# Optimization experiments

Hardware: AMD Instinct MI355X
Metric: run time of the kernel (lower is better)

## Reference

```python
import jax, jax.numpy as jnp
import numpy as np

B = 8          # batch samples (decomposition_permutations)
M = 100000     # points per sample
V = 100000     # coarse voxels for max-pool/unpool (stride scaler groups)


def setup_inputs() -> dict:
    key = jax.random.key(0)
    ks = jax.random.split(key, 6)
    N = B * M
    C_in, C = 128, 128
    fea = jax.random.normal(ks[0], (N, C_in), jnp.float32)
    W1 = jax.random.normal(ks[1], (C_in, C), jnp.float32) / np.sqrt(C_in).astype(np.float32)
    b1 = jnp.zeros((C,), jnp.float32)
    W2 = jax.random.normal(ks[2], (C, 1), jnp.float32) / np.sqrt(C).astype(np.float32)
    b2 = jnp.zeros((1,), jnp.float32)
    voxel_ids = jax.random.randint(ks[3], (N,), 0, V, jnp.int32)
    target_idx = jax.random.randint(ks[4], (N // 2,), 0, N, jnp.int32)
    return dict(fea=fea, W1=W1, b1=b1, W2=W2, b2=b2,
                voxel_ids=voxel_ids, target_idx=target_idx, target_num=M // 2)


def _get_keep(p, voxel_ids, target_num):
    # MinkowskiMaxPooling + PoolingTranspose diff: per-voxel max broadcast back
    local_max = jax.ops.segment_max(p, voxel_ids, num_segments=V)[voxel_ids]
    local_max_mask = p != local_max  # points NOT equal to their local max
    pm = p.reshape(B, M)
    mm = local_max_mask.reshape(B, M)
    # kthvalue over masked values per sample: k = M - target_num (1-indexed)
    vals = jnp.where(mm, pm, jnp.inf)          # non-masked pushed to the end
    k = M - target_num
    thr = jnp.sort(vals, axis=1)[:, k - 1]     # [B] per-sample thresholds
    keep = pm > thr[:, None]                   # BCE branch: keep pred > threshold
    keep = keep | ~mm                          # keep.logical_or_(~local_max_mask)
    return keep.reshape(B * M)


def reference(fea, W1, b1, W2, b2, voxel_ids, target_idx, target_num):
    # upsample_block -> classify_block
    h = jax.nn.relu(fea @ W1 + b1)             # [N, C]
    pred = h @ W2 + b2                         # [N, 1]
    p = pred[:, 0]
    keep = _get_keep(p, voxel_ids, target_num)
    # get_target: kernel_map scatter -> keep_target (training: keep |= keep_target)
    keep_target = jnp.zeros((p.shape[0],), bool).at[target_idx].set(True)
    keep = keep | keep_target
    # MinkowskiPruning (mask instead of compaction to keep shapes static)
    out = h * keep[:, None].astype(h.dtype)
    return out, pred, keep_target
```

## Files before the change

### kernel.cpp

```cpp
#include <hip/hip_runtime.h>
#include <stdint.h>

#define BATCH 8
#define C 128
#define TPB 256
#define GEMM_BLOCKS 512
#define TILE_R 128
#define HGRID 2048

__device__ __forceinline__ unsigned f2key(float f){
  unsigned b = __float_as_uint(f);
  return (b & 0x80000000u) ? ~b : (b | 0x80000000u);
}

__global__ __launch_bounds__(TPB, 1) void k_gemm(
    const float* __restrict__ fea, const float* __restrict__ W1,
    const float* __restrict__ b1, const float* __restrict__ W2,
    const float* __restrict__ b2, const int* __restrict__ vox,
    float* __restrict__ out, float* __restrict__ pred,
    unsigned* __restrict__ segkey, int N)
{
  __shared__ float sW1t[C * C];
  __shared__ double sPredS[2 * TILE_R];

  const int tid  = threadIdx.x;
  const int lane = tid & 63;
  const int wid  = tid >> 6;
  const int wr   = wid >> 1;
  const int wc   = wid & 1;
  const int rowoff = wr * 64 + (lane >> 3) * 8;
  const int coloff = wc * 64 + (lane & 7) * 8;
  const int lmask  = lane & 7;

  for (int idx = tid; idx < C * C; idx += TPB) {
    int k = idx >> 7, c = idx & 127;
    sW1t[c * C + (((k >> 2) ^ ((c >> 3) & 7)) << 2) + (k & 3)] = W1[idx];
  }
  float b1v[8];
  #pragma unroll
  for (int i = 0; i < 8; ++i) b1v[i] = b1[coloff + i];
  const double b2d = (double)b2[0];
  __syncthreads();

  const int nTiles = N / TILE_R;
  const float* bcol = &sW1t[coloff * C];

  for (int tile = blockIdx.x; tile < nTiles; tile += GEMM_BLOCKS) {
    const size_t trow = (size_t)tile * TILE_R;
    const float* abase = fea + (trow + rowoff) * C;

    float4 Aa[8], Ab[8];
    #pragma unroll
    for (int j = 0; j < 8; ++j) Aa[j] = *(const float4*)(abase + j * C);

    float acc[8][8];
    #pragma unroll
    for (int j = 0; j < 8; ++j)
      #pragma unroll
      for (int i = 0; i < 8; ++i) acc[j][i] = b1v[i];

    #pragma unroll 1
    for (int kg = 0; kg < 32; kg += 2) {
      #pragma unroll
      for (int j = 0; j < 8; ++j)
        Ab[j] = *(const float4*)(abase + j * C + (kg + 1) * 4);
      {
        const int goff = ((kg ^ lmask) << 2);
        float4 Bv[8];
        #pragma unroll
        for (int i = 0; i < 8; ++i)
          Bv[i] = *(const float4*)(bcol + i * C + goff);
        #pragma unroll
        for (int j = 0; j < 8; ++j) {
          #pragma unroll
          for (int i = 0; i < 8; ++i) acc[j][i] = fmaf(Aa[j].x, Bv[i].x, acc[j][i]);
          #pragma unroll
          for (int i = 0; i < 8; ++i) acc[j][i] = fmaf(Aa[j].y, Bv[i].y, acc[j][i]);
          #pragma unroll
          for (int i = 0; i < 8; ++i) acc[j][i] = fmaf(Aa[j].z, Bv[i].z, acc[j][i]);
          #pragma unroll
          for (int i = 0; i < 8; ++i) acc[j][i] = fmaf(Aa[j].w, Bv[i].w, acc[j][i]);
        }
      }
      if (kg + 2 < 32) {
        #pragma unroll
        for (int j = 0; j < 8; ++j)
          Aa[j] = *(const float4*)(abase + j * C + (kg + 2) * 4);
      }
      {
        const int goff = (((kg + 1) ^ lmask) << 2);
        float4 Bv[8];
        #pragma unroll
        for (int i = 0; i < 8; ++i)
          Bv[i] = *(const float4*)(bcol + i * C + goff);
        #pragma unroll
        for (int j = 0; j < 8; ++j) {
          #pragma unroll
          for (int i = 0; i < 8; ++i) acc[j][i] = fmaf(Ab[j].x, Bv[i].x, acc[j][i]);
          #pragma unroll
          for (int i = 0; i < 8; ++i) acc[j][i] = fmaf(Ab[j].y, Bv[i].y, acc[j][i]);
          #pragma unroll
          for (int i = 0; i < 8; ++i) acc[j][i] = fmaf(Ab[j].z, Bv[i].z, acc[j][i]);
          #pragma unroll
          for (int i = 0; i < 8; ++i) acc[j][i] = fmaf(Ab[j].w, Bv[i].w, acc[j][i]);
        }
      }
    }

    float w2f[8];
    #pragma unroll
    for (int i = 0; i < 8; ++i) w2f[i] = W2[coloff + i];
    double pdv[8];
    #pragma unroll
    for (int j = 0; j < 8; ++j) {
      float hv[8];
      #pragma unroll
      for (int i = 0; i < 8; ++i) hv[i] = fmaxf(acc[j][i], 0.f);
      const size_t row = trow + rowoff + j;
      *(float4*)(out + row * C + coloff)     = make_float4(hv[0], hv[1], hv[2], hv[3]);
      *(float4*)(out + row * C + coloff + 4) = make_float4(hv[4], hv[5], hv[6], hv[7]);
      double pd = 0.0;
      #pragma unroll
      for (int i = 0; i < 8; ++i) pd += (double)hv[i] * (double)w2f[i];
      pdv[j] = pd;
    }
    #pragma unroll
    for (int j = 0; j < 8; ++j) {
      double pd = pdv[j];
      pd += __shfl_xor(pd, 1, 64);
      pd += __shfl_xor(pd, 2, 64);
      pd += __shfl_xor(pd, 4, 64);
      pdv[j] = pd;
    }
    if ((lane & 7) == 0) {
      #pragma unroll
      for (int j = 0; j < 8; ++j) sPredS[wc * TILE_R + rowoff + j] = pdv[j];
    }
    __syncthreads();
    if (tid < TILE_R) {
      const double s = sPredS[tid] + sPredS[TILE_R + tid] + b2d;
      const float pv = (float)s;
      const size_t row = trow + tid;
      pred[row] = pv;
      atomicMax(&segkey[vox[row]], f2key(pv));
    }
    __syncthreads();
  }
}

__global__ __launch_bounds__(256) void k_histA(
    const float* __restrict__ pred, const int* __restrict__ vox,
    const unsigned* __restrict__ segkey, unsigned* __restrict__ valkey,
    unsigned* __restrict__ histA, int N, int M)
{
  __shared__ unsigned lh[BATCH * 256];
  for (int b = threadIdx.x; b < BATCH * 256; b += 256) lh[b] = 0;
  __syncthreads();
  const int stride = gridDim.x * 256;
  for (int i = blockIdx.x * 256 + threadIdx.x; i < N; i += stride) {
    unsigned kk = f2key(pred[i]);
    unsigned vk = (kk == segkey[vox[i]]) ? 0xFFFFFFFFu : kk;
    valkey[i] = vk;
    atomicAdd(&lh[(i / M) * 256 + (vk >> 24)], 1u);
  }
  __syncthreads();
  for (int b = threadIdx.x; b < BATCH * 256; b += 256)
    if (lh[b]) atomicAdd(&histA[b], lh[b]);
}

__global__ __launch_bounds__(256) void k_histB(
    const unsigned* __restrict__ valkey, const unsigned* __restrict__ sel,
    unsigned* __restrict__ histB, int N, int M)
{
  __shared__ unsigned lh[BATCH * 256];
  for (int b = threadIdx.x; b < BATCH * 256; b += 256) lh[b] = 0;
  __syncthreads();
  const int stride = gridDim.x * 256;
  for (int i = blockIdx.x * 256 + threadIdx.x; i < N; i += stride) {
    unsigned vk = valkey[i];
    int row = i / M;
    if ((vk >> 24) == sel[row * 4 + 0])
      atomicAdd(&lh[row * 256 + ((vk >> 16) & 255u)], 1u);
  }
  __syncthreads();
  for (int b = threadIdx.x; b < BATCH * 256; b += 256)
    if (lh[b]) atomicAdd(&histB[b], lh[b]);
}

__global__ __launch_bounds__(256) void k_histC(
    const unsigned* __restrict__ valkey, const unsigned* __restrict__ sel,
    unsigned* __restrict__ histC, int N, int M)
{
  const int stride = gridDim.x * 256;
  for (int i = blockIdx.x * 256 + threadIdx.x; i < N; i += stride) {
    unsigned vk = valkey[i];
    int row = i / M;
    if ((vk >> 16) == sel[row * 4 + 0])
      atomicAdd(&histC[(size_t)row * 65536 + (vk & 0xFFFFu)], 1u);
  }
}

__global__ void k_scan256(const unsigned* __restrict__ hist,
                          unsigned* __restrict__ sel,
                          const int* __restrict__ tnum, int M, int pass)
{
  const int row = blockIdx.x;
  __shared__ unsigned h[256];
  h[threadIdx.x] = hist[row * 256 + threadIdx.x];
  __syncthreads();
  if (threadIdx.x == 0) {
    const unsigned k = (unsigned)(M - tnum[0]);
    unsigned cum = (pass == 0) ? 0u : sel[row * 4 + 1];
    unsigned bin = 255;
    for (int i = 0; i < 256; ++i) {
      if (cum + h[i] >= k) { bin = (unsigned)i; break; }
      cum += h[i];
    }
    if (pass == 0) { sel[row * 4 + 0] = bin; }
    else           { sel[row * 4 + 0] = (sel[row * 4 + 0] << 8) | bin; }
    sel[row * 4 + 1] = cum;
  }
}

__global__ void k_scan64k(const unsigned* __restrict__ hist,
                          unsigned* __restrict__ sel,
                          const int* __restrict__ tnum, int M)
{
  const int row = blockIdx.x;
  const int t = threadIdx.x;
  const unsigned* h = hist + (size_t)row * 65536;
  __shared__ unsigned part[256];
  const uint4* hv = (const uint4*)(h + t * 256);
  unsigned s = 0;
  for (int i = 0; i < 64; ++i) { uint4 v = hv[i]; s += v.x + v.y + v.z + v.w; }
  part[t] = s;
  __syncthreads();
  if (t == 0) {
    const unsigned k = (unsigned)(M - tnum[0]);
    unsigned cum = sel[row * 4 + 1];
    int seg = 255;
    for (int i = 0; i < 256; ++i) {
      if (cum + part[i] >= k) { seg = i; break; }
      cum += part[i];
    }
    unsigned bin = 0;
    for (int i = 0; i < 256; ++i) {
      unsigned c = h[seg * 256 + i];
      if (cum + c >= k) { bin = (unsigned)(seg * 256 + i); break; }
      cum += c;
    }
    sel[row * 4 + 2] = (sel[row * 4 + 0] << 16) | bin;
  }
}

__global__ void k_scatter(const int* __restrict__ tidx, float* __restrict__ kt, int n)
{
  int i = blockIdx.x * blockDim.x + threadIdx.x;
  if (i < n) kt[tidx[i]] = 1.0f;
}

__global__ __launch_bounds__(256) void k_final(const unsigned* __restrict__ valkey,
    const float* __restrict__ kt, const unsigned* __restrict__ sel,
    float* __restrict__ out, int N, int M)
{
  const int wid = threadIdx.x >> 6;
  const int lane = threadIdx.x & 63;
  const int nw = gridDim.x * 4;
  for (int r = blockIdx.x * 4 + wid; r < N; r += nw) {
    unsigned vk = valkey[r];
    float kv = kt[r];
    unsigned thr = sel[(r / M) * 4 + 2];
    bool keep = (vk > thr) || (kv != 0.0f);
    if (!keep)
      *(float2*)&out[(size_t)r * C + lane * 2] = make_float2(0.f, 0.f);
  }
}

extern "C" void kernel_launch(void* const* d_in, const int* in_sizes, int n_in,
                              void* d_out, int out_size, void* d_ws, size_t ws_size,
                              hipStream_t stream)
{
  const float* fea = (const float*)d_in[0];
  const float* W1  = (const float*)d_in[1];
  const float* b1  = (const float*)d_in[2];
  const float* W2  = (const float*)d_in[3];
  const float* b2  = (const float*)d_in[4];
  const int* vox   = (const int*)d_in[5];
  const int* tidx  = (const int*)d_in[6];
  const int* tnum  = (const int*)d_in[7];

  const int N = in_sizes[5];
  const int M = N / BATCH;
  const int nT = in_sizes[6];

  float* out  = (float*)d_out;
  float* pred = out + (size_t)N * C;
  float* kt   = pred + N;

  char* w = (char*)d_ws;
  unsigned* segkey = (unsigned*)(w);
  unsigned* histA  = (unsigned*)(w + (512u << 10));
  unsigned* histB  = (unsigned*)(w + (520u << 10));
  unsigned* sel    = (unsigned*)(w + (528u << 10));
  unsigned* histC  = (unsigned*)(w + (532u << 10));
  unsigned* valkey = (unsigned*)(w + (532u << 10) + (2u << 20));

  const size_t zbytes = (532u << 10) + (2u << 20);
  hipMemsetAsync(d_ws, 0, zbytes, stream);
  hipMemsetAsync(kt, 0, (size_t)N * sizeof(float), stream);

  k_scatter<<<(nT + 255) / 256, 256, 0, stream>>>(tidx, kt, nT);
  k_gemm<<<GEMM_BLOCKS, TPB, 0, stream>>>(fea, W1, b1, W2, b2, vox,
                                          out, pred, segkey, N);
  k_histA<<<HGRID, 256, 0, stream>>>(pred, vox, segkey, valkey, histA, N, M);
  k_scan256<<<BATCH, 256, 0, stream>>>(histA, sel, tnum, M, 0);
  k_histB<<<HGRID, 256, 0, stream>>>(valkey, sel, histB, N, M);
  k_scan256<<<BATCH, 256, 0, stream>>>(histB, sel, tnum, M, 1);
  k_histC<<<HGRID, 256, 0, stream>>>(valkey, sel, histC, N, M);
  k_scan64k<<<BATCH, 256, 0, stream>>>(histC, sel, tnum, M);
  k_final<<<2048, 256, 0, stream>>>(valkey, kt, sel, out, N, M);
}
```

Measured before the change: 557.8 us.

## Split GEMM columns across block pairs and move pred reduction to separate kernel

Each GEMM block now handles one 64-column half of W1, which halves the shared memory per block, and the grid grows to 1024 blocks over 256-row tiles. The per-tile __syncthreads pair and the in-kernel cross-wave prediction reduction are removed. Each half writes partial double dot products to a workspace, and a new k_pred kernel sums them, adds the bias, and does the segment atomicMax. The aim is higher occupancy and no block-level barriers in the GEMM loop. The cost is that each fea row is read twice, by two blocks, and there is an extra kernel plus partial-sum traffic.

```diff
diff --git a/kernel.cpp b/kernel.cpp
--- a/kernel.cpp
+++ b/kernel.cpp
@@ -4,8 +4,8 @@
 #define BATCH 8
 #define C 128
 #define TPB 256
-#define GEMM_BLOCKS 512
-#define TILE_R 128
+#define GEMM_BLOCKS 1024
+#define TILE_R 256
 #define HGRID 2048
 
 __device__ __forceinline__ unsigned f2key(float f){
@@ -16,38 +16,37 @@
 __global__ __launch_bounds__(TPB, 1) void k_gemm(
     const float* __restrict__ fea, const float* __restrict__ W1,
     const float* __restrict__ b1, const float* __restrict__ W2,
-    const float* __restrict__ b2, const int* __restrict__ vox,
-    float* __restrict__ out, float* __restrict__ pred,
-    unsigned* __restrict__ segkey, int N)
-{
-  __shared__ float sW1t[C * C];
-  __shared__ double sPredS[2 * TILE_R];
+    const float* __restrict__ b2, float* __restrict__ out,
+    double* __restrict__ predpart, int N)
+{
+  __shared__ float sW1t[64 * C];
 
   const int tid  = threadIdx.x;
   const int lane = tid & 63;
   const int wid  = tid >> 6;
-  const int wr   = wid >> 1;
-  const int wc   = wid & 1;
-  const int rowoff = wr * 64 + (lane >> 3) * 8;
-  const int coloff = wc * 64 + (lane & 7) * 8;
+  const int half = blockIdx.x & 1;
+  const int clb  = (lane & 7) * 8;
+  const int coloff = half * 64 + clb;
+  const int rowloc = wid * 64 + (lane >> 3) * 8;
   const int lmask  = lane & 7;
 
-  for (int idx = tid; idx < C * C; idx += TPB) {
-    int k = idx >> 7, c = idx & 127;
-    sW1t[c * C + (((k >> 2) ^ ((c >> 3) & 7)) << 2) + (k & 3)] = W1[idx];
+  for (int idx = tid; idx < 64 * C; idx += TPB) {
+    int k = idx >> 6, cl = idx & 63;
+    sW1t[cl * C + (((k >> 2) ^ ((cl >> 3) & 7)) << 2) + (k & 3)] =
+        W1[k * C + half * 64 + cl];
   }
   float b1v[8];
   #pragma unroll
   for (int i = 0; i < 8; ++i) b1v[i] = b1[coloff + i];
-  const double b2d = (double)b2[0];
-  __syncthreads();
-
-  const int nTiles = N / TILE_R;
-  const float* bcol = &sW1t[coloff * C];
-
-  for (int tile = blockIdx.x; tile < nTiles; tile += GEMM_BLOCKS) {
+  __syncthreads();
+
+  const float* bcol = &sW1t[clb * C];
+  const int nJobs = (N / TILE_R) * 2;
+
+  for (int job = blockIdx.x; job < nJobs; job += GEMM_BLOCKS) {
+    const int tile = job >> 1;
     const size_t trow = (size_t)tile * TILE_R;
-    const float* abase = fea + (trow + rowoff) * C;
+    const float* abase = fea + (trow + rowloc) * C;
 
     float4 Aa[8], Ab[8];
     #pragma unroll
@@ -116,7 +115,7 @@
       float hv[8];
       #pragma unroll
       for (int i = 0; i < 8; ++i) hv[i] = fmaxf(acc[j][i], 0.f);
-      const size_t row = trow + rowoff + j;
+      const size_t row = trow + rowloc + j;
       *(float4*)(out + row * C + coloff)     = make_float4(hv[0], hv[1], hv[2], hv[3]);
       *(float4*)(out + row * C + coloff + 4) = make_float4(hv[4], hv[5], hv[6], hv[7]);
       double pd = 0.0;
@@ -134,18 +133,22 @@
     }
     if ((lane & 7) == 0) {
       #pragma unroll
-      for (int j = 0; j < 8; ++j) sPredS[wc * TILE_R + rowoff + j] = pdv[j];
-    }
-    __syncthreads();
-    if (tid < TILE_R) {
-      const double s = sPredS[tid] + sPredS[TILE_R + tid] + b2d;
-      const float pv = (float)s;
-      const size_t row = trow + tid;
-      pred[row] = pv;
-      atomicMax(&segkey[vox[row]], f2key(pv));
-    }
-    __syncthreads();
-  }
+      for (int j = 0; j < 8; ++j)
+        predpart[(size_t)half * N + trow + rowloc + j] = pdv[j];
+    }
+  }
+}
+
+__global__ __launch_bounds__(256) void k_pred(
+    const double* __restrict__ pp, const float* __restrict__ b2,
+    const int* __restrict__ vox, float* __restrict__ pred,
+    unsigned* __restrict__ segkey, int N)
+{
+  int i = blockIdx.x * 256 + threadIdx.x;
+  if (i >= N) return;
+  const float pv = (float)(pp[i] + pp[(size_t)N + i] + (double)b2[0]);
+  pred[i] = pv;
+  atomicMax(&segkey[vox[i]], f2key(pv));
 }
 
 __global__ __launch_bounds__(256) void k_histA(
@@ -304,14 +307,16 @@
   unsigned* sel    = (unsigned*)(w + (528u << 10));
   unsigned* histC  = (unsigned*)(w + (532u << 10));
   unsigned* valkey = (unsigned*)(w + (532u << 10) + (2u << 20));
+  double*  ppart   = (double*)(w + (532u << 10) + (2u << 20) + (size_t)N * 4);
 
   const size_t zbytes = (532u << 10) + (2u << 20);
   hipMemsetAsync(d_ws, 0, zbytes, stream);
   hipMemsetAsync(kt, 0, (size_t)N * sizeof(float), stream);
 
   k_scatter<<<(nT + 255) / 256, 256, 0, stream>>>(tidx, kt, nT);
-  k_gemm<<<GEMM_BLOCKS, TPB, 0, stream>>>(fea, W1, b1, W2, b2, vox,
-                                          out, pred, segkey, N);
+  k_gemm<<<GEMM_BLOCKS, TPB, 0, stream>>>(fea, W1, b1, W2, b2,
+                                          out, ppart, N);
+  k_pred<<<(N + 255) / 256, 256, 0, stream>>>(ppart, b2, vox, pred, segkey, N);
   k_histA<<<HGRID, 256, 0, stream>>>(pred, vox, segkey, valkey, histA, N, M);
   k_scan256<<<BATCH, 256, 0, stream>>>(histA, sel, tnum, M, 0);
   k_histB<<<HGRID, 256, 0, stream>>>(valkey, sel, histB, N, M);
```

New measurement: 608.0 us. 9.0% more time.
